# Performance work log

Measured on AMD Instinct MI355X. Metric: run time of the kernel, lower is better.

## Reference

```python
import jax, jax.numpy as jnp
import numpy as np
import math

B, S, D, H = 4, 2048, 1024, 16
DH = D // H  # per-head dim = 64
MASK_VAL = -1000000.0


def setup_inputs() -> dict:
    key = jax.random.key(0)
    ks = jax.random.split(key, 9)
    queries = jax.random.normal(ks[0], (B, S, D), dtype=jnp.float32)
    keys = jax.random.normal(ks[1], (B, S, D), dtype=jnp.float32)
    values = jax.random.normal(ks[2], (B, S, D), dtype=jnp.float32)
    valid_lens = jax.random.randint(ks[3], (B,), 0, S, dtype=jnp.int32)
    scale = 1.0 / math.sqrt(D)
    Wq = jax.random.normal(ks[4], (D, D), dtype=jnp.float32) * scale
    Wk = jax.random.normal(ks[5], (D, D), dtype=jnp.float32) * scale
    Wv = jax.random.normal(ks[6], (D, D), dtype=jnp.float32) * scale
    Wo = jax.random.normal(ks[7], (D, D), dtype=jnp.float32) * scale
    return {"queries": queries, "keys": keys, "values": values,
            "valid_lens": valid_lens, "Wq": Wq, "Wk": Wk, "Wv": Wv, "Wo": Wo}


def _split_heads(x):  # [B,S,D] -> [B,H,S,DH]
    b, s, _ = x.shape
    return x.reshape(b, s, H, DH).transpose(0, 2, 1, 3)


def reference(queries, keys, values, valid_lens, Wq, Wk, Wv, Wo):
    q = _split_heads(queries @ Wq)  # [B,H,S,DH]
    k = _split_heads(keys @ Wk)
    v = _split_heads(values @ Wv)
    scores = jnp.einsum('bhqd,bhkd->bhqk', q, k) / jnp.sqrt(jnp.float32(DH))
    # mask key positions >= valid_len[b] (sequence_mask with value=-1e6)
    key_pos = jnp.arange(S)  # [S]
    mask = key_pos[None, None, None, :] < valid_lens[:, None, None, None]  # [B,1,1,S]
    scores = jnp.where(mask, scores, MASK_VAL)
    attn = jax.nn.softmax(scores, axis=-1)  # [B,H,S,S] -- the 1GB intermediate
    out = jnp.einsum('bhqk,bhkd->bhqd', attn, v)  # [B,H,S,DH]
    out = out.transpose(0, 2, 1, 3).reshape(B, S, D)  # concat heads
    return out @ Wo
```

## Files before the change

### kernel.cpp

```cpp
#include <hip/hip_runtime.h>

#define BB 4
#define SS 2048
#define DD 1024
#define HH 16
#define DHH 64

typedef _Float16 half8 __attribute__((ext_vector_type(8)));
typedef _Float16 half4v __attribute__((ext_vector_type(4)));
typedef float floatx4 __attribute__((ext_vector_type(4)));

#define GLOBAL_AS __attribute__((address_space(1)))
#define LDS_AS __attribute__((address_space(3)))

__global__ void wt_kernel(const float* __restrict__ w0, const float* __restrict__ w1,
                          const float* __restrict__ w2, const float* __restrict__ w3,
                          _Float16* __restrict__ wt) {
  __shared__ float tile[32][33];
  int z = blockIdx.z;
  const float* w = (z == 0) ? w0 : (z == 1) ? w1 : (z == 2) ? w2 : w3;
  _Float16* dst = wt + (size_t)z * 1024 * 1024;
  int k0 = blockIdx.x * 32, n0 = blockIdx.y * 32;
  int tx = threadIdx.x & 31, ty = threadIdx.x >> 5;
#pragma unroll
  for (int r = ty; r < 32; r += 8) tile[r][tx] = w[(size_t)(k0 + r) * 1024 + n0 + tx];
  __syncthreads();
#pragma unroll
  for (int r = ty; r < 32; r += 8) dst[(size_t)(n0 + r) * 1024 + k0 + tx] = (_Float16)tile[tx][r];
}

__global__ void cvt3_kernel(const float* __restrict__ q, const float* __restrict__ k,
                            const float* __restrict__ v, _Float16* __restrict__ dst) {
  int z = blockIdx.y;
  const float* src = (z == 0) ? q : (z == 1) ? k : v;
  size_t i = ((size_t)blockIdx.x * 256 + threadIdx.x) * 8;
  float4 f0 = *(const float4*)(src + i);
  float4 f1 = *(const float4*)(src + i + 4);
  half8 h = {(_Float16)f0.x, (_Float16)f0.y, (_Float16)f0.z, (_Float16)f0.w,
             (_Float16)f1.x, (_Float16)f1.y, (_Float16)f1.z, (_Float16)f1.w};
  *(half8*)(dst + (size_t)z * 8388608 + i) = h;
}

__global__ __launch_bounds__(256) void qkv_gemm(const _Float16* __restrict__ Acat,
                                                const _Float16* __restrict__ Wt,
                                                _Float16* __restrict__ Qf,
                                                _Float16* __restrict__ Kf,
                                                _Float16* __restrict__ Vt) {
  __shared__ _Float16 lA[128 * 32];
  __shared__ _Float16 lB[128 * 32];
  int tid = threadIdx.x;
  int wave = tid >> 6, lane = tid & 63, quad = lane >> 4, l15 = lane & 15;
  int bn = blockIdx.x, bm = blockIdx.y;
  int proj = bm >> 6;
  int wm = wave >> 1, wn = wave & 1;

  const _Float16* A = Acat + (size_t)bm * 128 * 1024;
  const _Float16* W = Wt + (size_t)proj * 1024 * 1024;

  floatx4 fzero = {0.f, 0.f, 0.f, 0.f};
  floatx4 acc[4][4];
#pragma unroll
  for (int i = 0; i < 4; ++i)
#pragma unroll
    for (int j = 0; j < 4; ++j) acc[i][j] = fzero;

  int g0 = tid, g1 = 256 + tid;
  int row0 = g0 >> 2, gc0 = (g0 & 3) ^ ((row0 >> 1) & 3);
  int row1 = g1 >> 2, gc1 = (g1 & 3) ^ ((row1 >> 1) & 3);
  const _Float16* a0 = A + ((size_t)row0 * 1024 + gc0 * 8);
  const _Float16* a1 = A + ((size_t)row1 * 1024 + gc1 * 8);
  const _Float16* b0 = W + ((size_t)(bn * 128 + row0) * 1024 + gc0 * 8);
  const _Float16* b1 = W + ((size_t)(bn * 128 + row1) * 1024 + gc1 * 8);

  for (int k0 = 0; k0 < 1024; k0 += 32) {
    __builtin_amdgcn_global_load_lds((const GLOBAL_AS void*)(a0 + k0),
                                     (LDS_AS void*)(lA + g0 * 8), 16, 0, 0);
    __builtin_amdgcn_global_load_lds((const GLOBAL_AS void*)(a1 + k0),
                                     (LDS_AS void*)(lA + g1 * 8), 16, 0, 0);
    __builtin_amdgcn_global_load_lds((const GLOBAL_AS void*)(b0 + k0),
                                     (LDS_AS void*)(lB + g0 * 8), 16, 0, 0);
    __builtin_amdgcn_global_load_lds((const GLOBAL_AS void*)(b1 + k0),
                                     (LDS_AS void*)(lB + g1 * 8), 16, 0, 0);
    __syncthreads();

    half8 af[4], bf[4];
#pragma unroll
    for (int i = 0; i < 4; ++i) {
      int row = wm * 64 + i * 16 + l15;
      af[i] = *(const half8*)(lA + (row * 4 + (quad ^ ((row >> 1) & 3))) * 8);
    }
#pragma unroll
    for (int j = 0; j < 4; ++j) {
      int row = wn * 64 + j * 16 + l15;
      bf[j] = *(const half8*)(lB + (row * 4 + (quad ^ ((row >> 1) & 3))) * 8);
    }
#pragma unroll
    for (int i = 0; i < 4; ++i)
#pragma unroll
      for (int j = 0; j < 4; ++j)
        acc[i][j] = __builtin_amdgcn_mfma_f32_16x16x32_f16(af[i], bf[j], acc[i][j], 0, 0, 0);
    __syncthreads();
  }

  int rloc = (bm & 63) * 128;
#pragma unroll
  for (int i = 0; i < 4; ++i) {
#pragma unroll
    for (int j = 0; j < 4; ++j) {
      int rowb = rloc + wm * 64 + i * 16 + quad * 4;
      int col = bn * 128 + wn * 64 + j * 16 + l15;
      if (proj == 0) {
#pragma unroll
        for (int r = 0; r < 4; ++r)
          Qf[(size_t)(rowb + r) * 1024 + col] = (_Float16)(acc[i][j][r] * 0.125f);
      } else if (proj == 1) {
#pragma unroll
        for (int r = 0; r < 4; ++r)
          Kf[(size_t)(rowb + r) * 1024 + col] = (_Float16)acc[i][j][r];
      } else {
        int b = rowb >> 11, s = rowb & 2047;
        half4v pk = {(_Float16)acc[i][j][0], (_Float16)acc[i][j][1],
                     (_Float16)acc[i][j][2], (_Float16)acc[i][j][3]};
        *(half4v*)(Vt + (size_t)(b * 1024 + col) * 2048 + s) = pk;
      }
    }
  }
}

__global__ __launch_bounds__(256) void gemm_out(const _Float16* __restrict__ A,
                                                const _Float16* __restrict__ Wt,
                                                float* __restrict__ C) {
  __shared__ _Float16 lA[128 * 32];
  __shared__ _Float16 lB[128 * 32];
  int tid = threadIdx.x;
  int wave = tid >> 6, lane = tid & 63, quad = lane >> 4, l15 = lane & 15;
  int bn = blockIdx.x, bm = blockIdx.y;
  int wm = wave >> 1, wn = wave & 1;

  floatx4 fzero = {0.f, 0.f, 0.f, 0.f};
  floatx4 acc[4][4];
#pragma unroll
  for (int i = 0; i < 4; ++i)
#pragma unroll
    for (int j = 0; j < 4; ++j) acc[i][j] = fzero;

  int g0 = tid, g1 = 256 + tid;
  int row0 = g0 >> 2, gc0 = (g0 & 3) ^ ((row0 >> 1) & 3);
  int row1 = g1 >> 2, gc1 = (g1 & 3) ^ ((row1 >> 1) & 3);
  const _Float16* a0 = A + ((size_t)(bm * 128 + row0) * 1024 + gc0 * 8);
  const _Float16* a1 = A + ((size_t)(bm * 128 + row1) * 1024 + gc1 * 8);
  const _Float16* b0 = Wt + ((size_t)(bn * 128 + row0) * 1024 + gc0 * 8);
  const _Float16* b1 = Wt + ((size_t)(bn * 128 + row1) * 1024 + gc1 * 8);

  for (int k0 = 0; k0 < 1024; k0 += 32) {
    __builtin_amdgcn_global_load_lds((const GLOBAL_AS void*)(a0 + k0),
                                     (LDS_AS void*)(lA + g0 * 8), 16, 0, 0);
    __builtin_amdgcn_global_load_lds((const GLOBAL_AS void*)(a1 + k0),
                                     (LDS_AS void*)(lA + g1 * 8), 16, 0, 0);
    __builtin_amdgcn_global_load_lds((const GLOBAL_AS void*)(b0 + k0),
                                     (LDS_AS void*)(lB + g0 * 8), 16, 0, 0);
    __builtin_amdgcn_global_load_lds((const GLOBAL_AS void*)(b1 + k0),
                                     (LDS_AS void*)(lB + g1 * 8), 16, 0, 0);
    __syncthreads();

    half8 af[4], bf[4];
#pragma unroll
    for (int i = 0; i < 4; ++i) {
      int row = wm * 64 + i * 16 + l15;
      af[i] = *(const half8*)(lA + (row * 4 + (quad ^ ((row >> 1) & 3))) * 8);
    }
#pragma unroll
    for (int j = 0; j < 4; ++j) {
      int row = wn * 64 + j * 16 + l15;
      bf[j] = *(const half8*)(lB + (row * 4 + (quad ^ ((row >> 1) & 3))) * 8);
    }
#pragma unroll
    for (int i = 0; i < 4; ++i)
#pragma unroll
      for (int j = 0; j < 4; ++j)
        acc[i][j] = __builtin_amdgcn_mfma_f32_16x16x32_f16(af[i], bf[j], acc[i][j], 0, 0, 0);
    __syncthreads();
  }

#pragma unroll
  for (int i = 0; i < 4; ++i)
#pragma unroll
    for (int j = 0; j < 4; ++j) {
      int rowb = bm * 128 + wm * 64 + i * 16 + quad * 4;
      int col = bn * 128 + wn * 64 + j * 16 + l15;
#pragma unroll
      for (int r = 0; r < 4; ++r) C[(size_t)(rowb + r) * 1024 + col] = acc[i][j][r];
    }
}

__global__ __launch_bounds__(256) void attn_kernel(const _Float16* __restrict__ Q,
                                                   const _Float16* __restrict__ K,
                                                   const _Float16* __restrict__ Vt,
                                                   const int* __restrict__ vlens,
                                                   _Float16* __restrict__ O) {
  __shared__ _Float16 lK[64 * 64];
  __shared__ _Float16 lV[64 * 64];
  __shared__ _Float16 lP[4 * 16 * 64];

  int tid = threadIdx.x, wave = tid >> 6, lane = tid & 63, quad = lane >> 4, l15 = lane & 15;
  int bh = blockIdx.y, b = bh >> 4, h = bh & 15;
  int q0 = blockIdx.x * 64;
  int vlen = vlens[b];
  int nch = (vlen == 0) ? (SS / 64) : ((vlen + 63) >> 6);
  float mask_val = (vlen == 0) ? 0.0f : -1.0e6f;

  const _Float16* qb = Q + ((size_t)(b * SS + q0 + wave * 16 + l15) * DD + h * 64 + quad * 8);
  half8 qf0 = *(const half8*)qb;
  half8 qf1 = *(const half8*)(qb + 32);

  float l_part[4] = {0.f, 0.f, 0.f, 0.f};
  floatx4 fzero = {0.f, 0.f, 0.f, 0.f};
  floatx4 o[4];
#pragma unroll
  for (int j = 0; j < 4; ++j) o[j] = fzero;

  for (int kc = 0; kc < nch; ++kc) {
    int kb = kc * 64;
#pragma unroll
    for (int ss = tid; ss < 512; ss += 256) {
      int row = ss >> 3, gc = ss & 7;
      int sidx = (row * 8 + (gc ^ (row & 7))) * 8;
      *(half8*)(lK + sidx) =
          *(const half8*)(K + ((size_t)(b * SS + kb + row) * DD + h * 64 + gc * 8));
      *(half8*)(lV + sidx) =
          *(const half8*)(Vt + ((size_t)(b * DD + h * 64 + row) * SS + kb + gc * 8));
    }
    __syncthreads();

    floatx4 sacc[4];
#pragma unroll
    for (int j = 0; j < 4; ++j) sacc[j] = fzero;
#pragma unroll
    for (int ks = 0; ks < 2; ++ks) {
      half8 qf = ks ? qf1 : qf0;
#pragma unroll
      for (int j = 0; j < 4; ++j) {
        int row = j * 16 + l15, gc = ks * 4 + quad;
        half8 kf = *(const half8*)(lK + (row * 8 + (gc ^ (row & 7))) * 8);
        sacc[j] = __builtin_amdgcn_mfma_f32_16x16x32_f16(qf, kf, sacc[j], 0, 0, 0);
      }
    }

    bool clean = (kb + 64 <= vlen);
#pragma unroll
    for (int j = 0; j < 4; ++j) {
      int key = kb + j * 16 + l15;
      bool valid = clean | (key < vlen);
#pragma unroll
      for (int r = 0; r < 4; ++r) {
        float s = valid ? sacc[j][r] : mask_val;
        float p = __expf(s);
        l_part[r] += p;
        int row = quad * 4 + r, col = j * 16 + l15;
        int gc = col >> 3, off = col & 7;
        lP[wave * 1024 + row * 64 + (gc ^ (row & 7)) * 8 + off] = (_Float16)p;
      }
    }

#pragma unroll
    for (int ks = 0; ks < 2; ++ks) {
      int gc = ks * 4 + quad;
      half8 pf = *(const half8*)(lP + wave * 1024 + l15 * 64 + (gc ^ (l15 & 7)) * 8);
#pragma unroll
      for (int j = 0; j < 4; ++j) {
        int row = j * 16 + l15;
        half8 vf = *(const half8*)(lV + (row * 8 + (gc ^ (row & 7))) * 8);
        o[j] = __builtin_amdgcn_mfma_f32_16x16x32_f16(pf, vf, o[j], 0, 0, 0);
      }
    }
    __syncthreads();
  }

  float inv_l[4];
#pragma unroll
  for (int r = 0; r < 4; ++r) {
    float l = l_part[r];
#pragma unroll
    for (int off = 1; off < 16; off <<= 1) l += __shfl_xor(l, off);
    inv_l[r] = 1.0f / l;
  }
#pragma unroll
  for (int j = 0; j < 4; ++j) {
    int col = h * 64 + j * 16 + l15;
#pragma unroll
    for (int r = 0; r < 4; ++r) {
      int qrow = q0 + wave * 16 + quad * 4 + r;
      O[(size_t)(b * SS + qrow) * DD + col] = (_Float16)(o[j][r] * inv_l[r]);
    }
  }
}

extern "C" void kernel_launch(void* const* d_in, const int* in_sizes, int n_in,
                              void* d_out, int out_size, void* d_ws, size_t ws_size,
                              hipStream_t stream) {
  const float* q = (const float*)d_in[0];
  const float* k = (const float*)d_in[1];
  const float* v = (const float*)d_in[2];
  const int* vl = (const int*)d_in[3];
  const float* wq = (const float*)d_in[4];
  const float* wk = (const float*)d_in[5];
  const float* wv = (const float*)d_in[6];
  const float* wo = (const float*)d_in[7];

  char* ws = (char*)d_ws;
  _Float16* Wt = (_Float16*)ws;
  _Float16* Acat = (_Float16*)(ws + (8u << 20));
  _Float16* Qf = (_Float16*)(ws + (56u << 20));
  _Float16* Kf = (_Float16*)(ws + (72u << 20));
  _Float16* Vt = (_Float16*)(ws + (88u << 20));
  _Float16* Of = Acat;

  dim3 blk(256);

  wt_kernel<<<dim3(32, 32, 4), blk, 0, stream>>>(wq, wk, wv, wo, Wt);
  cvt3_kernel<<<dim3(4096, 3), blk, 0, stream>>>(q, k, v, Acat);
  qkv_gemm<<<dim3(8, 192), blk, 0, stream>>>(Acat, Wt, Qf, Kf, Vt);
  attn_kernel<<<dim3(32, 64), blk, 0, stream>>>(Qf, Kf, Vt, vl, Of);
  gemm_out<<<dim3(8, 64), blk, 0, stream>>>(Of, Wt + (3u << 20), (float*)d_out);
}
```

Measured before the change: 340.0 us.

## Merge prep kernels, enlarge attention Q tile, async K/V loads, retile output GEMM

The weight-transpose and input-convert kernels are merged into one launch, and the Q scale is folded into the Wq conversion. The attention kernel now processes 128 queries per block (32 per wave) so each K/V tile loaded into LDS is reused twice, and it loads K/V with direct global-to-LDS loads. The output GEMM uses 64x128 tiles to double the block count for better occupancy. The trade-offs are fewer attention blocks and higher register pressure from the doubled accumulators.

```diff
diff --git a/kernel.cpp b/kernel.cpp
--- a/kernel.cpp
+++ b/kernel.cpp
@@ -13,32 +13,37 @@
 #define GLOBAL_AS __attribute__((address_space(1)))
 #define LDS_AS __attribute__((address_space(3)))
 
-__global__ void wt_kernel(const float* __restrict__ w0, const float* __restrict__ w1,
-                          const float* __restrict__ w2, const float* __restrict__ w3,
-                          _Float16* __restrict__ wt) {
-  __shared__ float tile[32][33];
-  int z = blockIdx.z;
-  const float* w = (z == 0) ? w0 : (z == 1) ? w1 : (z == 2) ? w2 : w3;
-  _Float16* dst = wt + (size_t)z * 1024 * 1024;
-  int k0 = blockIdx.x * 32, n0 = blockIdx.y * 32;
-  int tx = threadIdx.x & 31, ty = threadIdx.x >> 5;
-#pragma unroll
-  for (int r = ty; r < 32; r += 8) tile[r][tx] = w[(size_t)(k0 + r) * 1024 + n0 + tx];
-  __syncthreads();
-#pragma unroll
-  for (int r = ty; r < 32; r += 8) dst[(size_t)(n0 + r) * 1024 + k0 + tx] = (_Float16)tile[tx][r];
-}
-
-__global__ void cvt3_kernel(const float* __restrict__ q, const float* __restrict__ k,
-                            const float* __restrict__ v, _Float16* __restrict__ dst) {
-  int z = blockIdx.y;
-  const float* src = (z == 0) ? q : (z == 1) ? k : v;
-  size_t i = ((size_t)blockIdx.x * 256 + threadIdx.x) * 8;
-  float4 f0 = *(const float4*)(src + i);
-  float4 f1 = *(const float4*)(src + i + 4);
-  half8 h = {(_Float16)f0.x, (_Float16)f0.y, (_Float16)f0.z, (_Float16)f0.w,
-             (_Float16)f1.x, (_Float16)f1.y, (_Float16)f1.z, (_Float16)f1.w};
-  *(half8*)(dst + (size_t)z * 8388608 + i) = h;
+__global__ void prep_kernel(const float* __restrict__ q, const float* __restrict__ k,
+                            const float* __restrict__ v, const float* __restrict__ wq,
+                            const float* __restrict__ wk, const float* __restrict__ wv,
+                            const float* __restrict__ wo, _Float16* __restrict__ wt,
+                            _Float16* __restrict__ acat) {
+  int bx = blockIdx.x;
+  if (bx < 4096) {
+    __shared__ float tile[32][33];
+    int z = bx >> 10, rem = bx & 1023;
+    const float* w = (z == 0) ? wq : (z == 1) ? wk : (z == 2) ? wv : wo;
+    float scale = (z == 0) ? 0.125f : 1.0f;
+    _Float16* dst = wt + (size_t)z * 1048576;
+    int k0 = (rem >> 5) * 32, n0 = (rem & 31) * 32;
+    int tx = threadIdx.x & 31, ty = threadIdx.x >> 5;
+#pragma unroll
+    for (int r = ty; r < 32; r += 8) tile[r][tx] = w[(size_t)(k0 + r) * 1024 + n0 + tx];
+    __syncthreads();
+#pragma unroll
+    for (int r = ty; r < 32; r += 8)
+      dst[(size_t)(n0 + r) * 1024 + k0 + tx] = (_Float16)(tile[tx][r] * scale);
+  } else {
+    int idx = bx - 4096;
+    int z = idx >> 12, xx = idx & 4095;
+    const float* src = (z == 0) ? q : (z == 1) ? k : v;
+    size_t i = ((size_t)xx * 256 + threadIdx.x) * 8;
+    float4 f0 = *(const float4*)(src + i);
+    float4 f1 = *(const float4*)(src + i + 4);
+    half8 h = {(_Float16)f0.x, (_Float16)f0.y, (_Float16)f0.z, (_Float16)f0.w,
+               (_Float16)f1.x, (_Float16)f1.y, (_Float16)f1.z, (_Float16)f1.w};
+    *(half8*)(acat + (size_t)z * 8388608 + i) = h;
+  }
 }
 
 __global__ __launch_bounds__(256) void qkv_gemm(const _Float16* __restrict__ Acat,
@@ -109,14 +114,11 @@
     for (int j = 0; j < 4; ++j) {
       int rowb = rloc + wm * 64 + i * 16 + quad * 4;
       int col = bn * 128 + wn * 64 + j * 16 + l15;
-      if (proj == 0) {
+      if (proj < 2) {
+        _Float16* dst = (proj == 0) ? Qf : Kf;
 #pragma unroll
         for (int r = 0; r < 4; ++r)
-          Qf[(size_t)(rowb + r) * 1024 + col] = (_Float16)(acc[i][j][r] * 0.125f);
-      } else if (proj == 1) {
-#pragma unroll
-        for (int r = 0; r < 4; ++r)
-          Kf[(size_t)(rowb + r) * 1024 + col] = (_Float16)acc[i][j][r];
+          dst[(size_t)(rowb + r) * 1024 + col] = (_Float16)acc[i][j][r];
       } else {
         int b = rowb >> 11, s = rowb & 2047;
         half4v pk = {(_Float16)acc[i][j][0], (_Float16)acc[i][j][1],
@@ -130,54 +132,51 @@
 __global__ __launch_bounds__(256) void gemm_out(const _Float16* __restrict__ A,
                                                 const _Float16* __restrict__ Wt,
                                                 float* __restrict__ C) {
-  __shared__ _Float16 lA[128 * 32];
+  __shared__ _Float16 lA[64 * 32];
   __shared__ _Float16 lB[128 * 32];
   int tid = threadIdx.x;
   int wave = tid >> 6, lane = tid & 63, quad = lane >> 4, l15 = lane & 15;
   int bn = blockIdx.x, bm = blockIdx.y;
-  int wm = wave >> 1, wn = wave & 1;
 
   floatx4 fzero = {0.f, 0.f, 0.f, 0.f};
-  floatx4 acc[4][4];
+  floatx4 acc[4][2];
 #pragma unroll
   for (int i = 0; i < 4; ++i)
 #pragma unroll
-    for (int j = 0; j < 4; ++j) acc[i][j] = fzero;
-
-  int g0 = tid, g1 = 256 + tid;
-  int row0 = g0 >> 2, gc0 = (g0 & 3) ^ ((row0 >> 1) & 3);
-  int row1 = g1 >> 2, gc1 = (g1 & 3) ^ ((row1 >> 1) & 3);
-  const _Float16* a0 = A + ((size_t)(bm * 128 + row0) * 1024 + gc0 * 8);
-  const _Float16* a1 = A + ((size_t)(bm * 128 + row1) * 1024 + gc1 * 8);
-  const _Float16* b0 = Wt + ((size_t)(bn * 128 + row0) * 1024 + gc0 * 8);
-  const _Float16* b1 = Wt + ((size_t)(bn * 128 + row1) * 1024 + gc1 * 8);
+    for (int j = 0; j < 2; ++j) acc[i][j] = fzero;
+
+  int ga = tid, gb0 = tid, gb1 = tid + 256;
+  int rowa = ga >> 2, gca = (ga & 3) ^ ((rowa >> 1) & 3);
+  int rowb0 = gb0 >> 2, gcb0 = (gb0 & 3) ^ ((rowb0 >> 1) & 3);
+  int rowb1 = gb1 >> 2, gcb1 = (gb1 & 3) ^ ((rowb1 >> 1) & 3);
+  const _Float16* a0 = A + ((size_t)(bm * 64 + rowa) * 1024 + gca * 8);
+  const _Float16* b0 = Wt + ((size_t)(bn * 128 + rowb0) * 1024 + gcb0 * 8);
+  const _Float16* b1 = Wt + ((size_t)(bn * 128 + rowb1) * 1024 + gcb1 * 8);
 
   for (int k0 = 0; k0 < 1024; k0 += 32) {
     __builtin_amdgcn_global_load_lds((const GLOBAL_AS void*)(a0 + k0),
-                                     (LDS_AS void*)(lA + g0 * 8), 16, 0, 0);
-    __builtin_amdgcn_global_load_lds((const GLOBAL_AS void*)(a1 + k0),
-                                     (LDS_AS void*)(lA + g1 * 8), 16, 0, 0);
+                                     (LDS_AS void*)(lA + ga * 8), 16, 0, 0);
     __builtin_amdgcn_global_load_lds((const GLOBAL_AS void*)(b0 + k0),
-                                     (LDS_AS void*)(lB + g0 * 8), 16, 0, 0);
+                                     (LDS_AS void*)(lB + gb0 * 8), 16, 0, 0);
     __builtin_amdgcn_global_load_lds((const GLOBAL_AS void*)(b1 + k0),
-                                     (LDS_AS void*)(lB + g1 * 8), 16, 0, 0);
-    __syncthreads();
-
-    half8 af[4], bf[4];
+                                     (LDS_AS void*)(lB + gb1 * 8), 16, 0, 0);
+    __syncthreads();
+
+    half8 af[4], bf[2];
 #pragma unroll
     for (int i = 0; i < 4; ++i) {
-      int row = wm * 64 + i * 16 + l15;
+      int row = i * 16 + l15;
       af[i] = *(const half8*)(lA + (row * 4 + (quad ^ ((row >> 1) & 3))) * 8);
     }
 #pragma unroll
-    for (int j = 0; j < 4; ++j) {
-      int row = wn * 64 + j * 16 + l15;
+    for (int j = 0; j < 2; ++j) {
+      int row = wave * 32 + j * 16 + l15;
       bf[j] = *(const half8*)(lB + (row * 4 + (quad ^ ((row >> 1) & 3))) * 8);
     }
 #pragma unroll
     for (int i = 0; i < 4; ++i)
 #pragma unroll
-      for (int j = 0; j < 4; ++j)
+      for (int j = 0; j < 2; ++j)
         acc[i][j] = __builtin_amdgcn_mfma_f32_16x16x32_f16(af[i], bf[j], acc[i][j], 0, 0, 0);
     __syncthreads();
   }
@@ -185,9 +184,9 @@
 #pragma unroll
   for (int i = 0; i < 4; ++i)
 #pragma unroll
-    for (int j = 0; j < 4; ++j) {
-      int rowb = bm * 128 + wm * 64 + i * 16 + quad * 4;
-      int col = bn * 128 + wn * 64 + j * 16 + l15;
+    for (int j = 0; j < 2; ++j) {
+      int rowb = bm * 64 + i * 16 + quad * 4;
+      int col = bn * 128 + wave * 32 + j * 16 + l15;
 #pragma unroll
       for (int r = 0; r < 4; ++r) C[(size_t)(rowb + r) * 1024 + col] = acc[i][j][r];
     }
@@ -200,49 +199,67 @@
                                                    _Float16* __restrict__ O) {
   __shared__ _Float16 lK[64 * 64];
   __shared__ _Float16 lV[64 * 64];
-  __shared__ _Float16 lP[4 * 16 * 64];
+  __shared__ _Float16 lP[4 * 32 * 64];
 
   int tid = threadIdx.x, wave = tid >> 6, lane = tid & 63, quad = lane >> 4, l15 = lane & 15;
   int bh = blockIdx.y, b = bh >> 4, h = bh & 15;
-  int q0 = blockIdx.x * 64;
+  int q0 = blockIdx.x * 128;
   int vlen = vlens[b];
   int nch = (vlen == 0) ? (SS / 64) : ((vlen + 63) >> 6);
   float mask_val = (vlen == 0) ? 0.0f : -1.0e6f;
 
-  const _Float16* qb = Q + ((size_t)(b * SS + q0 + wave * 16 + l15) * DD + h * 64 + quad * 8);
-  half8 qf0 = *(const half8*)qb;
-  half8 qf1 = *(const half8*)(qb + 32);
-
-  float l_part[4] = {0.f, 0.f, 0.f, 0.f};
+  half8 qf[2][2];
+#pragma unroll
+  for (int t = 0; t < 2; ++t) {
+    const _Float16* qb =
+        Q + ((size_t)(b * SS + q0 + wave * 32 + t * 16 + l15) * DD + h * 64 + quad * 8);
+    qf[t][0] = *(const half8*)qb;
+    qf[t][1] = *(const half8*)(qb + 32);
+  }
+
+  int g0 = tid, g1 = tid + 256;
+  int kr0 = g0 >> 3, kc0 = (g0 & 7) ^ (kr0 & 7);
+  int kr1 = g1 >> 3, kc1 = (g1 & 7) ^ (kr1 & 7);
+  const _Float16* ksrc0 = K + ((size_t)(b * SS + kr0) * DD + h * 64 + kc0 * 8);
+  const _Float16* ksrc1 = K + ((size_t)(b * SS + kr1) * DD + h * 64 + kc1 * 8);
+  const _Float16* vsrc0 = Vt + ((size_t)(b * DD + h * 64 + kr0) * SS + kc0 * 8);
+  const _Float16* vsrc1 = Vt + ((size_t)(b * DD + h * 64 + kr1) * SS + kc1 * 8);
+
+  float l_part[2][4] = {{0.f, 0.f, 0.f, 0.f}, {0.f, 0.f, 0.f, 0.f}};
   floatx4 fzero = {0.f, 0.f, 0.f, 0.f};
-  floatx4 o[4];
-#pragma unroll
-  for (int j = 0; j < 4; ++j) o[j] = fzero;
+  floatx4 o[2][4];
+#pragma unroll
+  for (int t = 0; t < 2; ++t)
+#pragma unroll
+    for (int j = 0; j < 4; ++j) o[t][j] = fzero;
 
   for (int kc = 0; kc < nch; ++kc) {
     int kb = kc * 64;
-#pragma unroll
-    for (int ss = tid; ss < 512; ss += 256) {
-      int row = ss >> 3, gc = ss & 7;
-      int sidx = (row * 8 + (gc ^ (row & 7))) * 8;
-      *(half8*)(lK + sidx) =
-          *(const half8*)(K + ((size_t)(b * SS + kb + row) * DD + h * 64 + gc * 8));
-      *(half8*)(lV + sidx) =
-          *(const half8*)(Vt + ((size_t)(b * DD + h * 64 + row) * SS + kb + gc * 8));
-    }
-    __syncthreads();
-
-    floatx4 sacc[4];
-#pragma unroll
-    for (int j = 0; j < 4; ++j) sacc[j] = fzero;
+    __builtin_amdgcn_global_load_lds((const GLOBAL_AS void*)(ksrc0 + (size_t)kb * DD),
+                                     (LDS_AS void*)(lK + g0 * 8), 16, 0, 0);
+    __builtin_amdgcn_global_load_lds((const GLOBAL_AS void*)(ksrc1 + (size_t)kb * DD),
+                                     (LDS_AS void*)(lK + g1 * 8), 16, 0, 0);
+    __builtin_amdgcn_global_load_lds((const GLOBAL_AS void*)(vsrc0 + kb),
+                                     (LDS_AS void*)(lV + g0 * 8), 16, 0, 0);
+    __builtin_amdgcn_global_load_lds((const GLOBAL_AS void*)(vsrc1 + kb),
+                                     (LDS_AS void*)(lV + g1 * 8), 16, 0, 0);
+    __syncthreads();
+
+    floatx4 sacc[2][4];
+#pragma unroll
+    for (int t = 0; t < 2; ++t)
+#pragma unroll
+      for (int j = 0; j < 4; ++j) sacc[t][j] = fzero;
 #pragma unroll
     for (int ks = 0; ks < 2; ++ks) {
-      half8 qf = ks ? qf1 : qf0;
+      int gc = ks * 4 + quad;
 #pragma unroll
       for (int j = 0; j < 4; ++j) {
-        int row = j * 16 + l15, gc = ks * 4 + quad;
+        int row = j * 16 + l15;
         half8 kf = *(const half8*)(lK + (row * 8 + (gc ^ (row & 7))) * 8);
-        sacc[j] = __builtin_amdgcn_mfma_f32_16x16x32_f16(qf, kf, sacc[j], 0, 0, 0);
+#pragma unroll
+        for (int t = 0; t < 2; ++t)
+          sacc[t][j] = __builtin_amdgcn_mfma_f32_16x16x32_f16(qf[t][ks], kf, sacc[t][j], 0, 0, 0);
       }
     }
 
@@ -252,47 +269,59 @@
       int key = kb + j * 16 + l15;
       bool valid = clean | (key < vlen);
 #pragma unroll
-      for (int r = 0; r < 4; ++r) {
-        float s = valid ? sacc[j][r] : mask_val;
-        float p = __expf(s);
-        l_part[r] += p;
-        int row = quad * 4 + r, col = j * 16 + l15;
-        int gc = col >> 3, off = col & 7;
-        lP[wave * 1024 + row * 64 + (gc ^ (row & 7)) * 8 + off] = (_Float16)p;
-      }
+      for (int t = 0; t < 2; ++t)
+#pragma unroll
+        for (int r = 0; r < 4; ++r) {
+          float s = valid ? sacc[t][j][r] : mask_val;
+          float p = __expf(s);
+          l_part[t][r] += p;
+          int row = t * 16 + quad * 4 + r, col = j * 16 + l15;
+          lP[wave * 2048 + row * 64 + ((col >> 3) ^ (row & 7)) * 8 + (col & 7)] = (_Float16)p;
+        }
     }
 
 #pragma unroll
     for (int ks = 0; ks < 2; ++ks) {
       int gc = ks * 4 + quad;
-      half8 pf = *(const half8*)(lP + wave * 1024 + l15 * 64 + (gc ^ (l15 & 7)) * 8);
+      half8 pf[2];
+#pragma unroll
+      for (int t = 0; t < 2; ++t) {
+        int prow = t * 16 + l15;
+        pf[t] = *(const half8*)(lP + wave * 2048 + prow * 64 + ((gc ^ (prow & 7))) * 8);
+      }
 #pragma unroll
       for (int j = 0; j < 4; ++j) {
         int row = j * 16 + l15;
         half8 vf = *(const half8*)(lV + (row * 8 + (gc ^ (row & 7))) * 8);
-        o[j] = __builtin_amdgcn_mfma_f32_16x16x32_f16(pf, vf, o[j], 0, 0, 0);
-      }
-    }
-    __syncthreads();
-  }
-
-  float inv_l[4];
-#pragma unroll
-  for (int r = 0; r < 4; ++r) {
-    float l = l_part[r];
-#pragma unroll
-    for (int off = 1; off < 16; off <<= 1) l += __shfl_xor(l, off);
-    inv_l[r] = 1.0f / l;
-  }
-#pragma unroll
-  for (int j = 0; j < 4; ++j) {
-    int col = h * 64 + j * 16 + l15;
+#pragma unroll
+        for (int t = 0; t < 2; ++t)
+          o[t][j] = __builtin_amdgcn_mfma_f32_16x16x32_f16(pf[t], vf, o[t][j], 0, 0, 0);
+      }
+    }
+    __syncthreads();
+  }
+
+  float inv_l[2][4];
+#pragma unroll
+  for (int t = 0; t < 2; ++t)
 #pragma unroll
     for (int r = 0; r < 4; ++r) {
-      int qrow = q0 + wave * 16 + quad * 4 + r;
-      O[(size_t)(b * SS + qrow) * DD + col] = (_Float16)(o[j][r] * inv_l[r]);
-    }
-  }
+      float l = l_part[t][r];
+#pragma unroll
+      for (int off = 1; off < 16; off <<= 1) l += __shfl_xor(l, off);
+      inv_l[t][r] = 1.0f / l;
+    }
+#pragma unroll
+  for (int t = 0; t < 2; ++t)
+#pragma unroll
+    for (int j = 0; j < 4; ++j) {
+      int col = h * 64 + j * 16 + l15;
+#pragma unroll
+      for (int r = 0; r < 4; ++r) {
+        int qrow = q0 + wave * 32 + t * 16 + quad * 4 + r;
+        O[(size_t)(b * SS + qrow) * DD + col] = (_Float16)(o[t][j][r] * inv_l[t][r]);
+      }
+    }
 }
 
 extern "C" void kernel_launch(void* const* d_in, const int* in_sizes, int n_in,
@@ -317,9 +346,8 @@
 
   dim3 blk(256);
 
-  wt_kernel<<<dim3(32, 32, 4), blk, 0, stream>>>(wq, wk, wv, wo, Wt);
-  cvt3_kernel<<<dim3(4096, 3), blk, 0, stream>>>(q, k, v, Acat);
+  prep_kernel<<<dim3(16384), blk, 0, stream>>>(q, k, v, wq, wk, wv, wo, Wt, Acat);
   qkv_gemm<<<dim3(8, 192), blk, 0, stream>>>(Acat, Wt, Qf, Kf, Vt);
-  attn_kernel<<<dim3(32, 64), blk, 0, stream>>>(Qf, Kf, Vt, vl, Of);
-  gemm_out<<<dim3(8, 64), blk, 0, stream>>>(Of, Wt + (3u << 20), (float*)d_out);
-}
+  attn_kernel<<<dim3(16, 64), blk, 0, stream>>>(Qf, Kf, Vt, vl, Of);
+  gemm_out<<<dim3(8, 128), blk, 0, stream>>>(Of, Wt + 3 * 1048576, (float*)d_out);
+}
```

New measurement: 357.2 us. +5.0%, slower.
